# Kernel optimization log

Hardware: AMD Instinct MI355X
Metric: run time of the kernel (lower is better)

## Reference

```python
import jax, jax.numpy as jnp
import numpy as np

NT, NC = 100000, 25000
ETT, ECT = 800000, 400000
DIN_T, DIN_C = 64, 32
H, C = 4, 32
HID = H * C  # 128
SLOPE = 0.2  # GATConv LeakyReLU negative slope


def setup_inputs() -> dict:
    key = jax.random.key(0)
    ks = jax.random.split(key, 24)
    def p(i, shape, s=0.05):
        return jax.random.normal(ks[i], shape, dtype=jnp.float32) * s
    return {
        'x_target': jax.random.normal(ks[0], (NT, DIN_T), dtype=jnp.float32),
        'x_context': jax.random.normal(ks[1], (NC, DIN_C), dtype=jnp.float32),
        'edge_tt': jax.random.randint(ks[2], (2, ETT), 0, NT),
        'edge_ct_src': jax.random.randint(ks[3], (ECT,), 0, NC),
        'edge_ct_dst': jax.random.randint(ks[4], (ECT,), 0, NT),
        'W_pre_t': p(5, (DIN_T, HID)), 'b_pre_t': jnp.zeros((HID,), jnp.float32),
        'W_pre_c': p(6, (DIN_C, HID)), 'b_pre_c': jnp.zeros((HID,), jnp.float32),
        'W_sd': p(7, (HID, HID)), 'att_src_sd': p(8, (H, C)), 'att_dst_sd': p(9, (H, C)), 'b_sd': jnp.zeros((HID,), jnp.float32),
        'W_ds': p(10, (HID, HID)), 'att_src_ds': p(11, (H, C)), 'att_dst_ds': p(12, (H, C)), 'b_ds': jnp.zeros((HID,), jnp.float32),
        'W_ct_src': p(13, (HID, HID)), 'W_ct_dst': p(14, (HID, HID)), 'att_src_ct': p(15, (H, C)), 'att_dst_ct': p(16, (H, C)), 'b_ct': jnp.zeros((HID,), jnp.float32),
        'W_out': p(17, (HID, HID)), 'b_out': jnp.zeros((HID,), jnp.float32),
    }


def _gat(h_src, h_dst, att_s, att_d, src, dst, n_dst, bias):
    # h_src: [N_src,H,C] transformed src feats; h_dst: [N_dst,H,C]
    a_s = jnp.einsum('nhc,hc->nh', h_src, att_s)  # [N_src,H]
    a_d = jnp.einsum('nhc,hc->nh', h_dst, att_d)  # [N_dst,H]
    e = a_s[src] + a_d[dst]                        # [E,H]
    e = jnp.where(e > 0, e, SLOPE * e)             # LeakyReLU(0.2)
    m = jax.ops.segment_max(e, dst, num_segments=n_dst)  # stable softmax per dst
    ex = jnp.exp(e - m[dst])
    den = jax.ops.segment_sum(ex, dst, num_segments=n_dst)
    alpha = ex / den[dst]                          # [E,H]
    msg = h_src[src] * alpha[:, :, None]           # [E,H,C]
    out = jax.ops.segment_sum(msg, dst, num_segments=n_dst)
    return out.reshape(n_dst, H * C) + bias


def reference(x_target, x_context, edge_tt, edge_ct_src, edge_ct_dst,
              W_pre_t, b_pre_t, W_pre_c, b_pre_c,
              W_sd, att_src_sd, att_dst_sd, b_sd,
              W_ds, att_src_ds, att_dst_ds, b_ds,
              W_ct_src, W_ct_dst, att_src_ct, att_dst_ct, b_ct,
              W_out, b_out):
    # HeteroDictLinear pretransform + relu
    h_t = jax.nn.relu(x_target @ W_pre_t + b_pre_t)   # [NT,128]
    h_c = jax.nn.relu(x_context @ W_pre_c + b_pre_c)  # [NC,128]
    res = h_t
    # DirGATConv on (target,to,target): forward + reversed, each w/ self-loops
    loops = jnp.arange(NT)
    src_f = jnp.concatenate([edge_tt[0], loops]); dst_f = jnp.concatenate([edge_tt[1], loops])
    src_r = jnp.concatenate([edge_tt[1], loops]); dst_r = jnp.concatenate([edge_tt[0], loops])
    hs = (h_t @ W_sd).reshape(NT, H, C)
    out_sd = _gat(hs, hs, att_src_sd, att_dst_sd, src_f, dst_f, NT, b_sd)
    hd = (h_t @ W_ds).reshape(NT, H, C)
    out_ds = _gat(hd, hd, att_src_ds, att_dst_ds, src_r, dst_r, NT, b_ds)
    out_tt = 0.5 * out_sd + 0.5 * out_ds  # (1-alpha), alpha with alpha=0.5
    # bipartite GATConv on (context,to,target), no self loops
    hcs = (h_c @ W_ct_src).reshape(NC, H, C)
    htd = (h_t @ W_ct_dst).reshape(NT, H, C)
    out_ct = _gat(hcs, htd, att_src_ct, att_dst_ct, edge_ct_src, edge_ct_dst, NT, b_ct)
    # HeteroConv aggr='mean' over the two edge types hitting 'target'
    x = 0.5 * (out_tt + out_ct)
    x = jax.nn.relu(x + res)  # skip connection + relu
    return x @ W_out + b_out
```

## Files before the change

### kernel.cpp

```cpp
#include <hip/hip_runtime.h>
#include <cstdint>
#include <cstddef>

typedef unsigned short u16;
typedef unsigned int u32;

#define NT 100000
#define NC 25000
#define ETT 800000
#define ECT 400000
#define SLOPE 0.2f
#define LOG2E 1.4426950408889634f
#define OFFS (NT + 4)

#define NBK 782
#define NBLK 256
#define CHT ((ETT + NBLK - 1) / NBLK)
#define CHC ((ECT + NBLK - 1) / NBLK)
#define TOTC (3 * NBK * NBLK)
#define NSB ((TOTC + 4095) / 4096)
#define FILL_CAP 4096

#define PT_BLK ((NT + 63) / 64)
#define CT_BLK ((NC + 63) / 64)

typedef __attribute__((ext_vector_type(8))) short bf16x8;
typedef __attribute__((ext_vector_type(4))) float f32x4;

__device__ __forceinline__ u16 f2bf(float f) {
  u32 u = __float_as_uint(f);
  u32 r = (u >> 16) & 1u;
  return (u16)((u + 0x7fffu + r) >> 16);
}
__device__ __forceinline__ float lof(u32 p) { return __uint_as_float(p << 16); }
__device__ __forceinline__ float hif(u32 p) { return __uint_as_float(p & 0xffff0000u); }

__device__ __forceinline__ void compute_bpre(const int* __restrict__ bsum, int* s_bpre) {
  const int t = threadIdx.x;
  const int v = (t < NSB) ? bsum[t] : 0;
  s_bpre[t] = v;
  __syncthreads();
  for (int d = 1; d < 256; d <<= 1) {
    const int u = (t >= d) ? s_bpre[t - d] : 0;
    __syncthreads();
    s_bpre[t] += u;
    __syncthreads();
  }
  const int incl = s_bpre[t];
  __syncthreads();
  s_bpre[t] = incl - v;
  __syncthreads();
}

__global__ __launch_bounds__(256) void transform_hist_kernel(
    const int* __restrict__ tt_src, const int* __restrict__ tt_dst,
    const int* __restrict__ ect_d, int* __restrict__ cntblk,
    const float* __restrict__ Wsd, const float* __restrict__ AsSd, const float* __restrict__ AdSd,
    const float* __restrict__ Wds, const float* __restrict__ AsDs, const float* __restrict__ AdDs,
    const float* __restrict__ Wout,
    u16* __restrict__ bf_sd, u16* __restrict__ bf_ds, u16* __restrict__ bf_out,
    const float* __restrict__ Wcd, const float* __restrict__ attD,
    const float* __restrict__ bsd, const float* __restrict__ bds, const float* __restrict__ bct,
    float* __restrict__ cbias,
    const float* __restrict__ x_t, const float* __restrict__ Wpt, const float* __restrict__ bpt,
    u16* __restrict__ h_t, float* __restrict__ aD,
    const float* __restrict__ x_c, const float* __restrict__ Wpc, const float* __restrict__ bpc,
    const float* __restrict__ Wcs, const float* __restrict__ attS,
    u16* __restrict__ hc_bf, float* __restrict__ aS_c)
{
  __shared__ __align__(16) char smem[51200];
  const int t = threadIdx.x;

  if (blockIdx.x < NBLK) {
    int* h = (int*)smem;
    const int b = blockIdx.x;
    for (int i = t; i < 3 * NBK; i += 256) h[i] = 0;
    __syncthreads();
    const int lo = b * CHT, hi = min(lo + CHT, ETT);
    for (int i = lo + t; i < hi; i += 256) {
      atomicAdd(&h[tt_dst[i] >> 7], 1);
      atomicAdd(&h[NBK + (tt_src[i] >> 7)], 1);
    }
    const int lo2 = b * CHC, hi2 = min(lo2 + CHC, ECT);
    for (int i = lo2 + t; i < hi2; i += 256)
      atomicAdd(&h[2 * NBK + (ect_d[i] >> 7)], 1);
    __syncthreads();
    for (int i = t; i < 3 * NBK; i += 256)
      cntblk[(size_t)i * NBLK + b] = h[i];
    return;
  }

  const int b = blockIdx.x - NBLK;

  if (b < 4) {
    if (b == 3) {
      if (t < 128) cbias[t] = 0.25f * bsd[t] + 0.25f * bds[t] + 0.5f * bct[t];
      return;
    }
    float* fS = (float*)smem;
    float* fD = fS + 512;
    const float* W = (b == 0) ? Wsd : (b == 1) ? Wds : Wout;
    const float* As = (b == 0) ? AsSd : AsDs;
    const float* Ad = (b == 0) ? AdSd : AdDs;
    u16* out = (b == 0) ? bf_sd : (b == 1) ? bf_ds : bf_out;
    const int tiles = (b == 2) ? 8 : 9;
    if (b < 2) {
      if (t < 128) {
        for (int hh = 0; hh < 4; ++hh) {
          float s1 = 0.f, s2 = 0.f;
          for (int c = 0; c < 32; ++c) {
            const float wv = W[t * 128 + hh * 32 + c];
            s1 = fmaf(wv, As[hh * 32 + c], s1);
            s2 = fmaf(wv, Ad[hh * 32 + c], s2);
          }
          fS[t * 4 + hh] = s1 * LOG2E; fD[t * 4 + hh] = s2 * LOG2E;
        }
      }
      __syncthreads();
    }
    const int total = tiles * 4 * 64 * 8;
    for (int i = t; i < total; i += 256) {
      const int j = i & 7, lane = (i >> 3) & 63, ks = (i >> 9) & 3, ti = i >> 11;
      const int k = ks * 32 + (lane >> 4) * 8 + j;
      const int n = ti * 16 + (lane & 15);
      float v;
      if (n < 128) v = W[k * 128 + n];
      else if (n < 132) v = fS[k * 4 + (n - 128)];
      else if (n < 136) v = fD[k * 4 + (n - 132)];
      else v = 0.f;
      out[i] = f2bf(v);
    }
    return;
  }

  if (b < 4 + PT_BLK) {
    float (*s_xt)[68] = (float(*)[68])smem;
    float (*s_W)[128] = (float(*)[128])(smem + 17408);
    float* s_fold     = (float*)(smem + 17408 + 16384);
    const int row0 = (b - 4) * 64;
    for (int g = 0; g < 4; ++g) {
      const int lr = g * 16 + (t >> 4);
      const int k4 = (t & 15) * 4;
      const int grow = row0 + lr;
      float4 f = make_float4(0.f, 0.f, 0.f, 0.f);
      if (grow < NT) f = *(const float4*)(x_t + (size_t)grow * 64 + k4);
      s_xt[k4 + 0][lr] = f.x; s_xt[k4 + 1][lr] = f.y;
      s_xt[k4 + 2][lr] = f.z; s_xt[k4 + 3][lr] = f.w;
    }
    if (t < 128) {
      for (int hh = 0; hh < 4; ++hh) {
        float s = 0.f;
        for (int c = 0; c < 32; ++c)
          s = fmaf(Wcd[t * 128 + hh * 32 + c], attD[hh * 32 + c], s);
        s_fold[t * 4 + hh] = s * LOG2E;
      }
    }
    const int rg = t >> 4;
    const int cg = t & 15;
    float acc[4][8];
    for (int r = 0; r < 4; ++r)
      for (int j = 0; j < 8; ++j)
        acc[r][j] = bpt[cg * 4 + (j & 3) + (j >> 2) * 64];
    for (int kc = 0; kc < 64; kc += 32) {
      for (int j = 0; j < 4; ++j) {
        const int idx = t + j * 256;
        const int k = idx >> 5, c4 = (idx & 31) * 4;
        *(float4*)&s_W[k][c4] = *(const float4*)(Wpt + (size_t)(kc + k) * 128 + c4);
      }
      __syncthreads();
#pragma unroll 8
      for (int k = 0; k < 32; ++k) {
        const float4 xa = *(const float4*)&s_xt[kc + k][rg * 4];
        const float4 w0 = *(const float4*)&s_W[k][cg * 4];
        const float4 w1 = *(const float4*)&s_W[k][cg * 4 + 64];
        const float xr[4] = {xa.x, xa.y, xa.z, xa.w};
        for (int r = 0; r < 4; ++r) {
          acc[r][0] = fmaf(xr[r], w0.x, acc[r][0]);
          acc[r][1] = fmaf(xr[r], w0.y, acc[r][1]);
          acc[r][2] = fmaf(xr[r], w0.z, acc[r][2]);
          acc[r][3] = fmaf(xr[r], w0.w, acc[r][3]);
          acc[r][4] = fmaf(xr[r], w1.x, acc[r][4]);
          acc[r][5] = fmaf(xr[r], w1.y, acc[r][5]);
          acc[r][6] = fmaf(xr[r], w1.z, acc[r][6]);
          acc[r][7] = fmaf(xr[r], w1.w, acc[r][7]);
        }
      }
      __syncthreads();
    }
    float4 fc0[2], fc1[2];
    fc0[0] = *(const float4*)&s_fold[(cg * 4 + 0) * 4];
    (void)fc0; (void)fc1;
    for (int r = 0; r < 4; ++r) {
      const int grow = row0 + rg * 4 + r;
      float v[8];
      for (int j = 0; j < 8; ++j) v[j] = fmaxf(acc[r][j], 0.f);
      float p0 = 0.f, p1 = 0.f, p2 = 0.f, p3 = 0.f;
      for (int j = 0; j < 8; ++j) {
        const int col = cg * 4 + (j & 3) + ((j >> 2) * 64);
        const float4 f4 = *(const float4*)&s_fold[col * 4];
        p0 = fmaf(v[j], f4.x, p0); p1 = fmaf(v[j], f4.y, p1);
        p2 = fmaf(v[j], f4.z, p2); p3 = fmaf(v[j], f4.w, p3);
      }
      if (grow < NT) {
        uint2 pk;
        pk.x = (u32)f2bf(v[0]) | ((u32)f2bf(v[1]) << 16);
        pk.y = (u32)f2bf(v[2]) | ((u32)f2bf(v[3]) << 16);
        *(uint2*)(h_t + (size_t)grow * 128 + cg * 4) = pk;
        pk.x = (u32)f2bf(v[4]) | ((u32)f2bf(v[5]) << 16);
        pk.y = (u32)f2bf(v[6]) | ((u32)f2bf(v[7]) << 16);
        *(uint2*)(h_t + (size_t)grow * 128 + cg * 4 + 64) = pk;
      }
      for (int m = 1; m < 16; m <<= 1) {
        p0 += __shfl_xor(p0, m); p1 += __shfl_xor(p1, m);
        p2 += __shfl_xor(p2, m); p3 += __shfl_xor(p3, m);
      }
      if (cg == 0 && grow < NT)
        *(float4*)(aD + (size_t)grow * 4) = make_float4(p0, p1, p2, p3);
    }
    return;
  }

  {
    float (*s_ht)[68]  = (float(*)[68])smem;
    float (*s_W2)[128] = (float(*)[128])(smem + 34816);
    float (*s_xc)[68]  = (float(*)[68])smem;
    const int row0 = (b - 4 - PT_BLK) * 64;
    for (int g = 0; g < 2; ++g) {
      const int lr = g * 32 + (t >> 3);
      const int k4 = (t & 7) * 4;
      const int grow = row0 + lr;
      float4 f = make_float4(0.f, 0.f, 0.f, 0.f);
      if (grow < NC) f = *(const float4*)(x_c + (size_t)grow * 32 + k4);
      s_xc[k4 + 0][lr] = f.x; s_xc[k4 + 1][lr] = f.y;
      s_xc[k4 + 2][lr] = f.z; s_xc[k4 + 3][lr] = f.w;
    }
    for (int j = 0; j < 4; ++j) {
      const int idx = t + j * 256;
      const int k = idx >> 5, c4 = (idx & 31) * 4;
      *(float4*)&s_W2[k][c4] = *(const float4*)(Wpc + (size_t)k * 128 + c4);
    }
    __syncthreads();
    const int rg = t >> 4, cg = t & 15;
    float acc1[4][8];
    for (int r = 0; r < 4; ++r)
      for (int j = 0; j < 8; ++j)
        acc1[r][j] = bpc[cg * 4 + (j & 3) + (j >> 2) * 64];
#pragma unroll 8
    for (int k = 0; k < 32; ++k) {
      const float4 xa = *(const float4*)&s_xc[k][rg * 4];
      const float4 w0 = *(const float4*)&s_W2[k][cg * 4];
      const float4 w1 = *(const float4*)&s_W2[k][cg * 4 + 64];
      const float xr[4] = {xa.x, xa.y, xa.z, xa.w};
      for (int r = 0; r < 4; ++r) {
        acc1[r][0] = fmaf(xr[r], w0.x, acc1[r][0]);
        acc1[r][1] = fmaf(xr[r], w0.y, acc1[r][1]);
        acc1[r][2] = fmaf(xr[r], w0.z, acc1[r][2]);
        acc1[r][3] = fmaf(xr[r], w0.w, acc1[r][3]);
        acc1[r][4] = fmaf(xr[r], w1.x, acc1[r][4]);
        acc1[r][5] = fmaf(xr[r], w1.y, acc1[r][5]);
        acc1[r][6] = fmaf(xr[r], w1.z, acc1[r][6]);
        acc1[r][7] = fmaf(xr[r], w1.w, acc1[r][7]);
      }
    }
    __syncthreads();
    for (int r = 0; r < 4; ++r) {
      const int lr = rg * 4 + r;
      for (int j = 0; j < 8; ++j) {
        const int col = cg * 4 + (j & 3) + ((j >> 2) * 64);
        s_ht[col][lr] = fmaxf(acc1[r][j], 0.f);
      }
    }
    for (int j = 0; j < 4; ++j) {
      const int idx = t + j * 256;
      const int k = idx >> 5, c4 = (idx & 31) * 4;
      *(float4*)&s_W2[k][c4] = *(const float4*)(Wcs + (size_t)k * 128 + c4);
    }
    __syncthreads();
    float acc2[4][8];
    for (int r = 0; r < 4; ++r)
      for (int j = 0; j < 8; ++j) acc2[r][j] = 0.f;
    for (int kc = 0; kc < 128; kc += 32) {
#pragma unroll 8
      for (int k = 0; k < 32; ++k) {
        const float4 xa = *(const float4*)&s_ht[kc + k][rg * 4];
        const float4 w0 = *(const float4*)&s_W2[k][cg * 4];
        const float4 w1 = *(const float4*)&s_W2[k][cg * 4 + 64];
        const float xr[4] = {xa.x, xa.y, xa.z, xa.w};
        for (int r = 0; r < 4; ++r) {
          acc2[r][0] = fmaf(xr[r], w0.x, acc2[r][0]);
          acc2[r][1] = fmaf(xr[r], w0.y, acc2[r][1]);
          acc2[r][2] = fmaf(xr[r], w0.z, acc2[r][2]);
          acc2[r][3] = fmaf(xr[r], w0.w, acc2[r][3]);
          acc2[r][4] = fmaf(xr[r], w1.x, acc2[r][4]);
          acc2[r][5] = fmaf(xr[r], w1.y, acc2[r][5]);
          acc2[r][6] = fmaf(xr[r], w1.z, acc2[r][6]);
          acc2[r][7] = fmaf(xr[r], w1.w, acc2[r][7]);
        }
      }
      if (kc < 96) {
        __syncthreads();
        for (int j = 0; j < 4; ++j) {
          const int idx = t + j * 256;
          const int k = idx >> 5, c4 = (idx & 31) * 4;
          *(float4*)&s_W2[k][c4] = *(const float4*)(Wcs + (size_t)(kc + 32 + k) * 128 + c4);
        }
        __syncthreads();
      }
    }
    const int h2 = cg >> 3;
    const float4 at0 = *(const float4*)(attS + cg * 4);
    const float4 at1 = *(const float4*)(attS + cg * 4 + 64);
    for (int r = 0; r < 4; ++r) {
      const int grow = row0 + rg * 4 + r;
      float pa = acc2[r][0] * at0.x + acc2[r][1] * at0.y +
                 acc2[r][2] * at0.z + acc2[r][3] * at0.w;
      float pb = acc2[r][4] * at1.x + acc2[r][5] * at1.y +
                 acc2[r][6] * at1.z + acc2[r][7] * at1.w;
      if (grow < NC) {
        uint2 pk;
        pk.x = (u32)f2bf(acc2[r][0]) | ((u32)f2bf(acc2[r][1]) << 16);
        pk.y = (u32)f2bf(acc2[r][2]) | ((u32)f2bf(acc2[r][3]) << 16);
        *(uint2*)(hc_bf + (size_t)grow * 128 + cg * 4) = pk;
        pk.x = (u32)f2bf(acc2[r][4]) | ((u32)f2bf(acc2[r][5]) << 16);
        pk.y = (u32)f2bf(acc2[r][6]) | ((u32)f2bf(acc2[r][7]) << 16);
        *(uint2*)(hc_bf + (size_t)grow * 128 + cg * 4 + 64) = pk;
      }
      for (int m = 1; m < 8; m <<= 1) {
        pa += __shfl_xor(pa, m);
        pb += __shfl_xor(pb, m);
      }
      if ((cg & 7) == 0 && grow < NC) {
        aS_c[(size_t)grow * 4 + h2] = pa * LOG2E;
        aS_c[(size_t)grow * 4 + 2 + h2] = pb * LOG2E;
      }
    }
  }
}

__global__ __launch_bounds__(256) void scan2_blk_kernel(const int* __restrict__ in,
    int* __restrict__ out, int* __restrict__ bsum)
{
  const int t = threadIdx.x, b = blockIdx.x;
  const int idx = b * 4096 + t * 16;
  int v[16];
  int s = 0;
  if (idx < TOTC) {
#pragma unroll
    for (int q = 0; q < 4; ++q) {
      const int4 qq = *(const int4*)(in + idx + q * 4);
      v[q * 4 + 0] = s; s += qq.x;
      v[q * 4 + 1] = s; s += qq.y;
      v[q * 4 + 2] = s; s += qq.z;
      v[q * 4 + 3] = s; s += qq.w;
    }
  } else {
    for (int j = 0; j < 16; ++j) v[j] = 0;
  }
  __shared__ int sh[256];
  sh[t] = s;
  __syncthreads();
  for (int d = 1; d < 256; d <<= 1) {
    const int u = (t >= d) ? sh[t - d] : 0;
    __syncthreads();
    sh[t] += u;
    __syncthreads();
  }
  const int excl = (t == 0) ? 0 : sh[t - 1];
  if (idx < TOTC) {
#pragma unroll
    for (int q = 0; q < 4; ++q) {
      int4 qo;
      qo.x = excl + v[q * 4 + 0]; qo.y = excl + v[q * 4 + 1];
      qo.z = excl + v[q * 4 + 2]; qo.w = excl + v[q * 4 + 3];
      *(int4*)(out + idx + q * 4) = qo;
    }
  }
  if (t == 255) bsum[b] = sh[255];
}

__global__ __launch_bounds__(256) void bin_logits2_kernel(
    const int* __restrict__ tt_src, const int* __restrict__ tt_dst,
    const int* __restrict__ ect_s, const int* __restrict__ ect_d,
    const int* __restrict__ scanned, const int* __restrict__ bsum, u32* __restrict__ bin,
    const short* __restrict__ A, const short* __restrict__ Bsd, const short* __restrict__ Bds,
    u16* __restrict__ hs, float* __restrict__ aSsd, float* __restrict__ aDsd,
    u16* __restrict__ hd, float* __restrict__ aSds, float* __restrict__ aDds, int M)
{
  __shared__ __align__(16) float ldsf[4][16][148];
  const int t = threadIdx.x;

  if (blockIdx.x < NBLK) {
    int* cur = (int*)&ldsf[0][0][0];
    int* s_bpre = cur + 3 * NBK;
    compute_bpre(bsum, s_bpre);
    const int b = blockIdx.x;
    for (int i = t; i < 3 * NBK; i += 256) {
      const int idx = i * NBLK + b;
      cur[i] = scanned[idx] + s_bpre[idx >> 12];
    }
    __syncthreads();
    const int lo = b * CHT, hi = min(lo + CHT, ETT);
    for (int i = lo + t; i < hi; i += 256) {
      const int s = tt_src[i], d = tt_dst[i];
      int p = atomicAdd(&cur[d >> 7], 1);
      bin[p] = ((u32)(d & 127) << 17) | (u32)s;
      p = atomicAdd(&cur[NBK + (s >> 7)], 1);
      bin[p] = ((u32)(s & 127) << 17) | (u32)d;
    }
    const int lo2 = b * CHC, hi2 = min(lo2 + CHC, ECT);
    for (int i = lo2 + t; i < hi2; i += 256) {
      const int s = ect_s[i], d = ect_d[i];
      const int p = atomicAdd(&cur[2 * NBK + (d >> 7)], 1);
      bin[p] = ((u32)(d & 127) << 17) | (u32)s;
    }
    return;
  }

  float (*lds)[16][148] = ldsf;
  const int blk = blockIdx.x - NBLK;
  const int wv = t >> 6, lane = t & 63;
  const int quad = lane >> 4, l16 = lane & 15;
  const int row0 = blk * 64 + wv * 16;
  const int arow = min(row0 + l16, M - 1);
  const short* ap = A + (size_t)arow * 128 + quad * 8;
  bf16x8 af[4];
  for (int ks = 0; ks < 4; ++ks) af[ks] = *(const bf16x8*)(ap + ks * 32);
  const int row = row0 + l16;
  const int idx = lane & 7, rr = lane >> 3;
  for (int pass = 0; pass < 2; ++pass) {
    const short* B = pass ? Bds : Bsd;
    u16* outb = pass ? hd : hs;
    float* aS = pass ? aSds : aSsd;
    float* aD = pass ? aDds : aDsd;
    f32x4 acc[9];
    for (int ti = 0; ti < 9; ++ti) acc[ti] = (f32x4){0.f, 0.f, 0.f, 0.f};
    for (int ks = 0; ks < 4; ++ks)
      for (int ti = 0; ti < 9; ++ti) {
        const bf16x8 bf = *(const bf16x8*)(B + ((ti * 4 + ks) * 64 + lane) * 8);
        acc[ti] = __builtin_amdgcn_mfma_f32_16x16x32_bf16(af[ks], bf, acc[ti], 0, 0, 0);
      }
    for (int ti = 0; ti < 9; ++ti)
      for (int r = 0; r < 4; ++r)
        lds[wv][quad * 4 + r][ti * 16 + l16] = acc[ti][r];
    __syncthreads();
    if (row < M) {
      for (int g = 0; g < 8; ++g) {
        const f32x4 v = *(const f32x4*)&lds[wv][l16][g * 16 + quad * 4];
        uint2 pk;
        pk.x = (u32)f2bf(v[0]) | ((u32)f2bf(v[1]) << 16);
        pk.y = (u32)f2bf(v[2]) | ((u32)f2bf(v[3]) << 16);
        *(uint2*)(outb + (size_t)row * 128 + g * 16 + quad * 4) = pk;
      }
    }
    for (int p = 0; p < 2; ++p) {
      const int lr = p * 8 + rr;
      const int n = row0 + lr;
      if (n < M) {
        const float v = lds[wv][lr][128 + idx];
        if (idx < 4) aS[(size_t)n * 4 + idx] = v;
        else aD[(size_t)n * 4 + idx - 4] = v;
      }
    }
    __syncthreads();
  }
}

__global__ __launch_bounds__(256) void bucket_fill_kernel(const int* __restrict__ scanned,
    const int* __restrict__ bsum, const u32* __restrict__ bin,
    int* __restrict__ offs, int* __restrict__ big_el)
{
  __shared__ int s_cnt[128], s_exc[128], s_cur[128], s_bpre[256];
  __shared__ int s_el[FILL_CAP];
  const int t = threadIdx.x;
  compute_bpre(bsum, s_bpre);
  const int rel = blockIdx.x / NBK;
  const int bucket = blockIdx.x - rel * NBK;
  if (t < 128) s_cnt[t] = 0;
  const int bi = blockIdx.x * NBLK;
  const int base = scanned[bi] + s_bpre[bi >> 12];
  const int nxt = (blockIdx.x == 3 * NBK - 1)
                      ? (2 * ETT + ECT)
                      : scanned[bi + NBLK] + s_bpre[(bi + NBLK) >> 12];
  __syncthreads();
  const int size = nxt - base;
  for (int i = t; i < size; i += 256)
    atomicAdd(&s_cnt[bin[base + i] >> 17], 1);
  __syncthreads();
  if (t < 128) s_exc[t] = s_cnt[t];
  __syncthreads();
  for (int d = 1; d < 128; d <<= 1) {
    int v = 0;
    if (t < 128 && t >= d) v = s_exc[t - d];
    __syncthreads();
    if (t < 128) s_exc[t] += v;
    __syncthreads();
  }
  const int relbase = rel * ETT;
  const int obase = base - relbase;
  int* off_rel = offs + (size_t)rel * OFFS;
  const int node0 = bucket * 128;
  if (t < 128) {
    const int excl = s_exc[t] - s_cnt[t];
    s_cur[t] = excl;
    if (node0 + t < NT) off_rel[node0 + t] = obase + excl;
  }
  if (t == 0 && bucket == NBK - 1) off_rel[NT] = obase + size;
  __syncthreads();
  int* el_rel = big_el + relbase;
  if (size <= FILL_CAP) {
    for (int i = t; i < size; i += 256) {
      const u32 e = bin[base + i];
      const int pos = atomicAdd(&s_cur[e >> 17], 1);
      s_el[pos] = (int)(e & 0x1FFFFu);
    }
    __syncthreads();
    for (int i = t; i < size; i += 256)
      el_rel[obase + i] = s_el[i];
  } else {
    for (int i = t; i < size; i += 256) {
      const u32 e = bin[base + i];
      const int pos = atomicAdd(&s_cur[e >> 17], 1);
      el_rel[obase + pos] = (int)(e & 0x1FFFFu);
    }
  }
}

__global__ __launch_bounds__(256) void mfma_out_kernel(
    const short* __restrict__ A, const short* __restrict__ B,
    const float* __restrict__ bias, float* __restrict__ out, int M)
{
  __shared__ __align__(16) float lds[4][16][132];
  const int wv = threadIdx.x >> 6, lane = threadIdx.x & 63;
  const int quad = lane >> 4, l16 = lane & 15;
  const int row0 = blockIdx.x * 64 + wv * 16;
  const int arow = min(row0 + l16, M - 1);
  const short* ap = A + (size_t)arow * 128 + quad * 8;
  bf16x8 af[4];
  for (int ks = 0; ks < 4; ++ks) af[ks] = *(const bf16x8*)(ap + ks * 32);
  f32x4 acc[8];
  for (int t = 0; t < 8; ++t) acc[t] = (f32x4){0.f, 0.f, 0.f, 0.f};
  for (int ks = 0; ks < 4; ++ks)
    for (int t = 0; t < 8; ++t) {
      const bf16x8 bf = *(const bf16x8*)(B + ((t * 4 + ks) * 64 + lane) * 8);
      acc[t] = __builtin_amdgcn_mfma_f32_16x16x32_bf16(af[ks], bf, acc[t], 0, 0, 0);
    }
  for (int t = 0; t < 8; ++t)
    for (int r = 0; r < 4; ++r)
      lds[wv][quad * 4 + r][t * 16 + l16] = acc[t][r];
  __syncthreads();
  const int row = row0 + l16;
  if (row < M) {
    for (int g = 0; g < 8; ++g) {
      const int col = g * 16 + quad * 4;
      f32x4 v = *(const f32x4*)&lds[wv][l16][col];
      const f32x4 b4 = *(const f32x4*)(bias + col);
      v = v + b4;
      *(f32x4*)(out + (size_t)row * 128 + col) = v;
    }
  }
}

__device__ __forceinline__ void gat_pipe16(const int* __restrict__ off,
    const int* __restrict__ el, const float* __restrict__ aS, const float* __restrict__ aD,
    const u16* __restrict__ hb, int d, int h, int cb, int self_loop, float w,
    float* __restrict__ acc)
{
  const float ad = aD[(size_t)d * 4 + h];
  const int beg = off[d];
  const int m = off[d + 1] - beg;
  const int cnt = m + self_loop;
  if (cnt <= 0) return;
  float den = 0.f;
  float a0 = 0.f, a1 = 0.f, a2 = 0.f, a3 = 0.f, a4 = 0.f, a5 = 0.f, a6 = 0.f, a7 = 0.f;
  int sB = (1 < m) ? el[beg + 1] : d;
  {
    const int sA0 = (0 < m) ? el[beg] : d;
    float eA = aS[(size_t)sA0 * 4 + h];
    uint4 pA = *(const uint4*)(hb + (size_t)sA0 * 128 + cb);
    for (int k = 0; k < cnt; ++k) {
      const int sC = (k + 2 < m) ? el[beg + k + 2] : d;
      const float eB = aS[(size_t)sB * 4 + h];
      const uint4 pB = *(const uint4*)(hb + (size_t)sB * 128 + cb);
      float ea = eA + ad;
      ea = ea > 0.f ? ea : SLOPE * ea;
      const float ex = exp2f(ea);
      den += ex;
      a0 = fmaf(ex, lof(pA.x), a0); a1 = fmaf(ex, hif(pA.x), a1);
      a2 = fmaf(ex, lof(pA.y), a2); a3 = fmaf(ex, hif(pA.y), a3);
      a4 = fmaf(ex, lof(pA.z), a4); a5 = fmaf(ex, hif(pA.z), a5);
      a6 = fmaf(ex, lof(pA.w), a6); a7 = fmaf(ex, hif(pA.w), a7);
      eA = eB; pA = pB; sB = sC;
    }
  }
  const float s = w / den;
  acc[0] = fmaf(a0, s, acc[0]); acc[1] = fmaf(a1, s, acc[1]);
  acc[2] = fmaf(a2, s, acc[2]); acc[3] = fmaf(a3, s, acc[3]);
  acc[4] = fmaf(a4, s, acc[4]); acc[5] = fmaf(a5, s, acc[5]);
  acc[6] = fmaf(a6, s, acc[6]); acc[7] = fmaf(a7, s, acc[7]);
}

__global__ __launch_bounds__(256) void gather_all_kernel(
    const int* __restrict__ off_f, const int* __restrict__ el_f,
    const float* __restrict__ aS_sd, const float* __restrict__ aD_sd, const u16* __restrict__ hs,
    const int* __restrict__ off_r, const int* __restrict__ el_r,
    const float* __restrict__ aS_ds, const float* __restrict__ aD_ds, const u16* __restrict__ hd,
    const int* __restrict__ off_c, const int* __restrict__ el_c,
    const float* __restrict__ aS_ct, const float* __restrict__ aD_ct, const u16* __restrict__ hc,
    const u16* __restrict__ skip, const float* __restrict__ cbias, u16* __restrict__ x)
{
  const int d = blockIdx.x * 16 + (threadIdx.x >> 4);
  if (d >= NT) return;
  const int lg = threadIdx.x & 15;
  const int h = lg >> 2;
  const int cb = lg * 8;
  float acc[8];
  for (int i = 0; i < 8; ++i) acc[i] = 0.f;
  gat_pipe16(off_f, el_f, aS_sd, aD_sd, hs, d, h, cb, 1, 0.25f, acc);
  gat_pipe16(off_r, el_r, aS_ds, aD_ds, hd, d, h, cb, 1, 0.25f, acc);
  gat_pipe16(off_c, el_c, aS_ct, aD_ct, hc, d, h, cb, 0, 0.5f, acc);
  const uint4 sk = *(const uint4*)(skip + (size_t)d * 128 + cb);
  const float4 cb0 = *(const float4*)(cbias + cb);
  const float4 cb1 = *(const float4*)(cbias + cb + 4);
  const float o0 = fmaxf(acc[0] + cb0.x + lof(sk.x), 0.f);
  const float o1 = fmaxf(acc[1] + cb0.y + hif(sk.x), 0.f);
  const float o2 = fmaxf(acc[2] + cb0.z + lof(sk.y), 0.f);
  const float o3 = fmaxf(acc[3] + cb0.w + hif(sk.y), 0.f);
  const float o4 = fmaxf(acc[4] + cb1.x + lof(sk.z), 0.f);
  const float o5 = fmaxf(acc[5] + cb1.y + hif(sk.z), 0.f);
  const float o6 = fmaxf(acc[6] + cb1.z + lof(sk.w), 0.f);
  const float o7 = fmaxf(acc[7] + cb1.w + hif(sk.w), 0.f);
  uint4 r;
  r.x = (u32)f2bf(o0) | ((u32)f2bf(o1) << 16);
  r.y = (u32)f2bf(o2) | ((u32)f2bf(o3) << 16);
  r.z = (u32)f2bf(o4) | ((u32)f2bf(o5) << 16);
  r.w = (u32)f2bf(o6) | ((u32)f2bf(o7) << 16);
  *(uint4*)(x + (size_t)d * 128 + cb) = r;
}

extern "C" void kernel_launch(void* const* d_in, const int* in_sizes, int n_in,
                              void* d_out, int out_size, void* d_ws, size_t ws_size,
                              hipStream_t stream)
{
  const float* x_t   = (const float*)d_in[0];
  const float* x_c   = (const float*)d_in[1];
  const int*   e_tt  = (const int*)d_in[2];
  const int*   ect_s = (const int*)d_in[3];
  const int*   ect_d = (const int*)d_in[4];
  const float* Wpt = (const float*)d_in[5];   const float* bpt = (const float*)d_in[6];
  const float* Wpc = (const float*)d_in[7];   const float* bpc = (const float*)d_in[8];
  const float* Wsd = (const float*)d_in[9];   const float* As_sd = (const float*)d_in[10];
  const float* Ad_sd = (const float*)d_in[11]; const float* bsd = (const float*)d_in[12];
  const float* Wds = (const float*)d_in[13];  const float* As_ds = (const float*)d_in[14];
  const float* Ad_ds = (const float*)d_in[15]; const float* bds = (const float*)d_in[16];
  const float* Wcs = (const float*)d_in[17];  const float* Wcd = (const float*)d_in[18];
  const float* As_ct = (const float*)d_in[19]; const float* Ad_ct = (const float*)d_in[20];
  const float* bct = (const float*)d_in[21];
  const float* Wout = (const float*)d_in[22]; const float* bout = (const float*)d_in[23];

  char* p = (char*)d_ws;
  size_t off = 0;
  auto alloc = [&](size_t bytes) { char* r = p + off; off += (bytes + 255) & ~(size_t)255; return r; };
  u16* ht_bf   = (u16*)alloc((size_t)NT * 128 * 2);
  u16* hs_bf   = (u16*)alloc((size_t)NT * 128 * 2);
  u16* hd_bf   = (u16*)alloc((size_t)NT * 128 * 2);
  u16* hc_bf   = (u16*)alloc((size_t)NC * 128 * 2);
  u16* x_bf    = (u16*)alloc((size_t)NT * 128 * 2);
  float* aS_sd = (float*)alloc((size_t)NT * 4 * 4);
  float* aD_sd = (float*)alloc((size_t)NT * 4 * 4);
  float* aS_ds = (float*)alloc((size_t)NT * 4 * 4);
  float* aD_ds = (float*)alloc((size_t)NT * 4 * 4);
  float* aS_ct = (float*)alloc((size_t)NC * 4 * 4);
  float* aD_ct = (float*)alloc((size_t)NT * 4 * 4);
  int* cntblk  = (int*)alloc((size_t)TOTC * 4);
  int* scanned = (int*)alloc((size_t)TOTC * 4);
  u32* bin     = (u32*)alloc((size_t)(2 * ETT + ECT) * 4);
  int* big_el  = (int*)alloc((size_t)(2 * ETT + ECT) * 4);
  int* offs    = (int*)alloc((size_t)3 * OFFS * 4);
  int* bsum    = (int*)alloc((size_t)NSB * 4);
  float* cbias   = (float*)alloc(128 * 4);
  u16* bfrag_sd  = (u16*)alloc((size_t)9 * 4 * 64 * 8 * 2);
  u16* bfrag_ds  = (u16*)alloc((size_t)9 * 4 * 64 * 8 * 2);
  u16* bfrag_out = (u16*)alloc((size_t)8 * 4 * 64 * 8 * 2);

  int* off_f = offs;
  int* off_r = offs + OFFS;
  int* off_c = offs + 2 * OFFS;
  int* el_f = big_el;
  int* el_r = big_el + ETT;
  int* el_c = big_el + 2 * ETT;

  const int* tt_src = e_tt;
  const int* tt_dst = e_tt + ETT;

  const int gM = (NT + 63) / 64;

  transform_hist_kernel<<<NBLK + 4 + PT_BLK + CT_BLK, 256, 0, stream>>>(
      tt_src, tt_dst, ect_d, cntblk,
      Wsd, As_sd, Ad_sd, Wds, As_ds, Ad_ds, Wout,
      bfrag_sd, bfrag_ds, bfrag_out,
      Wcd, Ad_ct, bsd, bds, bct, cbias,
      x_t, Wpt, bpt, ht_bf, aD_ct,
      x_c, Wpc, bpc, Wcs, As_ct, hc_bf, aS_ct);

  scan2_blk_kernel<<<NSB, 256, 0, stream>>>(cntblk, scanned, bsum);

  bin_logits2_kernel<<<NBLK + gM, 256, 0, stream>>>(
      tt_src, tt_dst, ect_s, ect_d, scanned, bsum, bin,
      (const short*)ht_bf, (const short*)bfrag_sd, (const short*)bfrag_ds,
      hs_bf, aS_sd, aD_sd, hd_bf, aS_ds, aD_ds, NT);

  bucket_fill_kernel<<<3 * NBK, 256, 0, stream>>>(scanned, bsum, bin, offs, big_el);

  gather_all_kernel<<<(NT + 15) / 16, 256, 0, stream>>>(
      off_f, el_f, aS_sd, aD_sd, hs_bf,
      off_r, el_r, aS_ds, aD_ds, hd_bf,
      off_c, el_c, aS_ct, aD_ct, hc_bf,
      ht_bf, cbias, x_bf);

  mfma_out_kernel<<<gM, 256, 0, stream>>>((const short*)x_bf, (const short*)bfrag_out,
                                          bout, (float*)d_out, NT);
}
```

Before: 375.7 us.

## Shrink LDS in transform kernel, halve context tiles, drop LDS from output GEMM

Cuts the transform kernel's shared memory from 51200 to 27648 bytes. It does this by streaming weights in 16-row K chunks and processing context nodes in 32-row tiles instead of 64, which should let more blocks fit per CU. The output MFMA kernel now writes accumulators straight to global memory with the bias added, instead of staging them through LDS with a barrier. The trade-offs are more syncthreads per block, twice as many context blocks, and narrower strided stores in the output kernel.

```diff
diff --git a/kernel.cpp b/kernel.cpp
--- a/kernel.cpp
+++ b/kernel.cpp
@@ -22,7 +22,8 @@
 #define FILL_CAP 4096
 
 #define PT_BLK ((NT + 63) / 64)
-#define CT_BLK ((NC + 63) / 64)
+#define CT_BLK ((NC + 31) / 32)
+#define GM_BLK ((NT + 63) / 64)
 
 typedef __attribute__((ext_vector_type(8))) short bf16x8;
 typedef __attribute__((ext_vector_type(4))) float f32x4;
@@ -68,7 +69,7 @@
     const float* __restrict__ Wcs, const float* __restrict__ attS,
     u16* __restrict__ hc_bf, float* __restrict__ aS_c)
 {
-  __shared__ __align__(16) char smem[51200];
+  __shared__ __align__(16) char smem[27648];
   const int t = threadIdx.x;
 
   if (blockIdx.x < NBLK) {
@@ -136,7 +137,7 @@
   if (b < 4 + PT_BLK) {
     float (*s_xt)[68] = (float(*)[68])smem;
     float (*s_W)[128] = (float(*)[128])(smem + 17408);
-    float* s_fold     = (float*)(smem + 17408 + 16384);
+    float* s_fold     = (float*)(smem + 17408 + 8192);
     const int row0 = (b - 4) * 64;
     for (int g = 0; g < 4; ++g) {
       const int lr = g * 16 + (t >> 4);
@@ -161,15 +162,15 @@
     for (int r = 0; r < 4; ++r)
       for (int j = 0; j < 8; ++j)
         acc[r][j] = bpt[cg * 4 + (j & 3) + (j >> 2) * 64];
-    for (int kc = 0; kc < 64; kc += 32) {
-      for (int j = 0; j < 4; ++j) {
+    for (int kc = 0; kc < 64; kc += 16) {
+      for (int j = 0; j < 2; ++j) {
         const int idx = t + j * 256;
         const int k = idx >> 5, c4 = (idx & 31) * 4;
         *(float4*)&s_W[k][c4] = *(const float4*)(Wpt + (size_t)(kc + k) * 128 + c4);
       }
       __syncthreads();
-#pragma unroll 8
-      for (int k = 0; k < 32; ++k) {
+#pragma unroll
+      for (int k = 0; k < 16; ++k) {
         const float4 xa = *(const float4*)&s_xt[kc + k][rg * 4];
         const float4 w0 = *(const float4*)&s_W[k][cg * 4];
         const float4 w1 = *(const float4*)&s_W[k][cg * 4 + 64];
@@ -187,9 +188,6 @@
       }
       __syncthreads();
     }
-    float4 fc0[2], fc1[2];
-    fc0[0] = *(const float4*)&s_fold[(cg * 4 + 0) * 4];
-    (void)fc0; (void)fc1;
     for (int r = 0; r < 4; ++r) {
       const int grow = row0 + rg * 4 + r;
       float v[8];
@@ -221,12 +219,12 @@
   }
 
   {
-    float (*s_ht)[68]  = (float(*)[68])smem;
-    float (*s_W2)[128] = (float(*)[128])(smem + 34816);
-    float (*s_xc)[68]  = (float(*)[68])smem;
-    const int row0 = (b - 4 - PT_BLK) * 64;
-    for (int g = 0; g < 2; ++g) {
-      const int lr = g * 32 + (t >> 3);
+    float (*s_ht)[36]  = (float(*)[36])smem;
+    float (*s_W2)[128] = (float(*)[128])(smem + 18432);
+    float (*s_xc)[36]  = (float(*)[36])smem;
+    const int row0 = (b - 4 - PT_BLK) * 32;
+    {
+      const int lr = t >> 3;
       const int k4 = (t & 7) * 4;
       const int grow = row0 + lr;
       float4 f = make_float4(0.f, 0.f, 0.f, 0.f);
@@ -234,59 +232,61 @@
       s_xc[k4 + 0][lr] = f.x; s_xc[k4 + 1][lr] = f.y;
       s_xc[k4 + 2][lr] = f.z; s_xc[k4 + 3][lr] = f.w;
     }
-    for (int j = 0; j < 4; ++j) {
-      const int idx = t + j * 256;
-      const int k = idx >> 5, c4 = (idx & 31) * 4;
-      *(float4*)&s_W2[k][c4] = *(const float4*)(Wpc + (size_t)k * 128 + c4);
-    }
-    __syncthreads();
     const int rg = t >> 4, cg = t & 15;
-    float acc1[4][8];
-    for (int r = 0; r < 4; ++r)
+    float acc1[2][8];
+    for (int r = 0; r < 2; ++r)
       for (int j = 0; j < 8; ++j)
         acc1[r][j] = bpc[cg * 4 + (j & 3) + (j >> 2) * 64];
-#pragma unroll 8
-    for (int k = 0; k < 32; ++k) {
-      const float4 xa = *(const float4*)&s_xc[k][rg * 4];
-      const float4 w0 = *(const float4*)&s_W2[k][cg * 4];
-      const float4 w1 = *(const float4*)&s_W2[k][cg * 4 + 64];
-      const float xr[4] = {xa.x, xa.y, xa.z, xa.w};
-      for (int r = 0; r < 4; ++r) {
-        acc1[r][0] = fmaf(xr[r], w0.x, acc1[r][0]);
-        acc1[r][1] = fmaf(xr[r], w0.y, acc1[r][1]);
-        acc1[r][2] = fmaf(xr[r], w0.z, acc1[r][2]);
-        acc1[r][3] = fmaf(xr[r], w0.w, acc1[r][3]);
-        acc1[r][4] = fmaf(xr[r], w1.x, acc1[r][4]);
-        acc1[r][5] = fmaf(xr[r], w1.y, acc1[r][5]);
-        acc1[r][6] = fmaf(xr[r], w1.z, acc1[r][6]);
-        acc1[r][7] = fmaf(xr[r], w1.w, acc1[r][7]);
-      }
-    }
-    __syncthreads();
-    for (int r = 0; r < 4; ++r) {
-      const int lr = rg * 4 + r;
+    for (int kc = 0; kc < 32; kc += 16) {
+      for (int j = 0; j < 2; ++j) {
+        const int idx = t + j * 256;
+        const int k = idx >> 5, c4 = (idx & 31) * 4;
+        *(float4*)&s_W2[k][c4] = *(const float4*)(Wpc + (size_t)(kc + k) * 128 + c4);
+      }
+      __syncthreads();
+#pragma unroll
+      for (int k = 0; k < 16; ++k) {
+        const float2 xa = *(const float2*)&s_xc[kc + k][rg * 2];
+        const float4 w0 = *(const float4*)&s_W2[k][cg * 4];
+        const float4 w1 = *(const float4*)&s_W2[k][cg * 4 + 64];
+        const float xr[2] = {xa.x, xa.y};
+        for (int r = 0; r < 2; ++r) {
+          acc1[r][0] = fmaf(xr[r], w0.x, acc1[r][0]);
+          acc1[r][1] = fmaf(xr[r], w0.y, acc1[r][1]);
+          acc1[r][2] = fmaf(xr[r], w0.z, acc1[r][2]);
+          acc1[r][3] = fmaf(xr[r], w0.w, acc1[r][3]);
+          acc1[r][4] = fmaf(xr[r], w1.x, acc1[r][4]);
+          acc1[r][5] = fmaf(xr[r], w1.y, acc1[r][5]);
+          acc1[r][6] = fmaf(xr[r], w1.z, acc1[r][6]);
+          acc1[r][7] = fmaf(xr[r], w1.w, acc1[r][7]);
+        }
+      }
+      __syncthreads();
+    }
+    for (int r = 0; r < 2; ++r) {
+      const int lr = rg * 2 + r;
       for (int j = 0; j < 8; ++j) {
         const int col = cg * 4 + (j & 3) + ((j >> 2) * 64);
         s_ht[col][lr] = fmaxf(acc1[r][j], 0.f);
       }
     }
-    for (int j = 0; j < 4; ++j) {
-      const int idx = t + j * 256;
-      const int k = idx >> 5, c4 = (idx & 31) * 4;
-      *(float4*)&s_W2[k][c4] = *(const float4*)(Wcs + (size_t)k * 128 + c4);
-    }
-    __syncthreads();
-    float acc2[4][8];
-    for (int r = 0; r < 4; ++r)
+    float acc2[2][8];
+    for (int r = 0; r < 2; ++r)
       for (int j = 0; j < 8; ++j) acc2[r][j] = 0.f;
-    for (int kc = 0; kc < 128; kc += 32) {
-#pragma unroll 8
-      for (int k = 0; k < 32; ++k) {
-        const float4 xa = *(const float4*)&s_ht[kc + k][rg * 4];
+    for (int kc = 0; kc < 128; kc += 16) {
+      for (int j = 0; j < 2; ++j) {
+        const int idx = t + j * 256;
+        const int k = idx >> 5, c4 = (idx & 31) * 4;
+        *(float4*)&s_W2[k][c4] = *(const float4*)(Wcs + (size_t)(kc + k) * 128 + c4);
+      }
+      __syncthreads();
+#pragma unroll
+      for (int k = 0; k < 16; ++k) {
+        const float2 xa = *(const float2*)&s_ht[kc + k][rg * 2];
         const float4 w0 = *(const float4*)&s_W2[k][cg * 4];
         const float4 w1 = *(const float4*)&s_W2[k][cg * 4 + 64];
-        const float xr[4] = {xa.x, xa.y, xa.z, xa.w};
-        for (int r = 0; r < 4; ++r) {
+        const float xr[2] = {xa.x, xa.y};
+        for (int r = 0; r < 2; ++r) {
           acc2[r][0] = fmaf(xr[r], w0.x, acc2[r][0]);
           acc2[r][1] = fmaf(xr[r], w0.y, acc2[r][1]);
           acc2[r][2] = fmaf(xr[r], w0.z, acc2[r][2]);
@@ -297,21 +297,13 @@
           acc2[r][7] = fmaf(xr[r], w1.w, acc2[r][7]);
         }
       }
-      if (kc < 96) {
-        __syncthreads();
-        for (int j = 0; j < 4; ++j) {
-          const int idx = t + j * 256;
-          const int k = idx >> 5, c4 = (idx & 31) * 4;
-          *(float4*)&s_W2[k][c4] = *(const float4*)(Wcs + (size_t)(kc + 32 + k) * 128 + c4);
-        }
-        __syncthreads();
-      }
+      __syncthreads();
     }
     const int h2 = cg >> 3;
     const float4 at0 = *(const float4*)(attS + cg * 4);
     const float4 at1 = *(const float4*)(attS + cg * 4 + 64);
-    for (int r = 0; r < 4; ++r) {
-      const int grow = row0 + rg * 4 + r;
+    for (int r = 0; r < 2; ++r) {
+      const int grow = row0 + rg * 2 + r;
       float pa = acc2[r][0] * at0.x + acc2[r][1] * at0.y +
                  acc2[r][2] * at0.z + acc2[r][3] * at0.w;
       float pb = acc2[r][4] * at1.x + acc2[r][5] * at1.y +
@@ -378,46 +370,12 @@
   if (t == 255) bsum[b] = sh[255];
 }
 
-__global__ __launch_bounds__(256) void bin_logits2_kernel(
-    const int* __restrict__ tt_src, const int* __restrict__ tt_dst,
-    const int* __restrict__ ect_s, const int* __restrict__ ect_d,
-    const int* __restrict__ scanned, const int* __restrict__ bsum, u32* __restrict__ bin,
+__device__ __forceinline__ void logits2_body(float (*lds)[16][148], int blk,
     const short* __restrict__ A, const short* __restrict__ Bsd, const short* __restrict__ Bds,
     u16* __restrict__ hs, float* __restrict__ aSsd, float* __restrict__ aDsd,
     u16* __restrict__ hd, float* __restrict__ aSds, float* __restrict__ aDds, int M)
 {
-  __shared__ __align__(16) float ldsf[4][16][148];
   const int t = threadIdx.x;
-
-  if (blockIdx.x < NBLK) {
-    int* cur = (int*)&ldsf[0][0][0];
-    int* s_bpre = cur + 3 * NBK;
-    compute_bpre(bsum, s_bpre);
-    const int b = blockIdx.x;
-    for (int i = t; i < 3 * NBK; i += 256) {
-      const int idx = i * NBLK + b;
-      cur[i] = scanned[idx] + s_bpre[idx >> 12];
-    }
-    __syncthreads();
-    const int lo = b * CHT, hi = min(lo + CHT, ETT);
-    for (int i = lo + t; i < hi; i += 256) {
-      const int s = tt_src[i], d = tt_dst[i];
-      int p = atomicAdd(&cur[d >> 7], 1);
-      bin[p] = ((u32)(d & 127) << 17) | (u32)s;
-      p = atomicAdd(&cur[NBK + (s >> 7)], 1);
-      bin[p] = ((u32)(s & 127) << 17) | (u32)d;
-    }
-    const int lo2 = b * CHC, hi2 = min(lo2 + CHC, ECT);
-    for (int i = lo2 + t; i < hi2; i += 256) {
-      const int s = ect_s[i], d = ect_d[i];
-      const int p = atomicAdd(&cur[2 * NBK + (d >> 7)], 1);
-      bin[p] = ((u32)(d & 127) << 17) | (u32)s;
-    }
-    return;
-  }
-
-  float (*lds)[16][148] = ldsf;
-  const int blk = blockIdx.x - NBLK;
   const int wv = t >> 6, lane = t & 63;
   const int quad = lane >> 4, l16 = lane & 15;
   const int row0 = blk * 64 + wv * 16;
@@ -463,6 +421,47 @@
     }
     __syncthreads();
   }
+}
+
+__global__ __launch_bounds__(256) void bin_logits2_kernel(
+    const int* __restrict__ tt_src, const int* __restrict__ tt_dst,
+    const int* __restrict__ ect_s, const int* __restrict__ ect_d,
+    const int* __restrict__ scanned, const int* __restrict__ bsum, u32* __restrict__ bin,
+    const short* __restrict__ A, const short* __restrict__ Bsd, const short* __restrict__ Bds,
+    u16* __restrict__ hs, float* __restrict__ aSsd, float* __restrict__ aDsd,
+    u16* __restrict__ hd, float* __restrict__ aSds, float* __restrict__ aDds, int M)
+{
+  __shared__ __align__(16) float ldsf[4][16][148];
+  const int t = threadIdx.x;
+
+  if (blockIdx.x < NBLK) {
+    int* cur = (int*)&ldsf[0][0][0];
+    int* s_bpre = cur + 3 * NBK;
+    compute_bpre(bsum, s_bpre);
+    const int b = blockIdx.x;
+    for (int i = t; i < 3 * NBK; i += 256) {
+      const int idx = i * NBLK + b;
+      cur[i] = scanned[idx] + s_bpre[idx >> 12];
+    }
+    __syncthreads();
+    const int lo = b * CHT, hi = min(lo + CHT, ETT);
+    for (int i = lo + t; i < hi; i += 256) {
+      const int s = tt_src[i], d = tt_dst[i];
+      int p = atomicAdd(&cur[d >> 7], 1);
+      bin[p] = ((u32)(d & 127) << 17) | (u32)s;
+      p = atomicAdd(&cur[NBK + (s >> 7)], 1);
+      bin[p] = ((u32)(s & 127) << 17) | (u32)d;
+    }
+    const int lo2 = b * CHC, hi2 = min(lo2 + CHC, ECT);
+    for (int i = lo2 + t; i < hi2; i += 256) {
+      const int s = ect_s[i], d = ect_d[i];
+      const int p = atomicAdd(&cur[2 * NBK + (d >> 7)], 1);
+      bin[p] = ((u32)(d & 127) << 17) | (u32)s;
+    }
+    return;
+  }
+  logits2_body(ldsf, blockIdx.x - NBLK, A, Bsd, Bds,
+               hs, aSsd, aDsd, hd, aSds, aDds, M);
 }
 
 __global__ __launch_bounds__(256) void bucket_fill_kernel(const int* __restrict__ scanned,
@@ -529,33 +528,32 @@
     const short* __restrict__ A, const short* __restrict__ B,
     const float* __restrict__ bias, float* __restrict__ out, int M)
 {
-  __shared__ __align__(16) float lds[4][16][132];
-  const int wv = threadIdx.x >> 6, lane = threadIdx.x & 63;
+  const int t = threadIdx.x;
+  const int wv = t >> 6, lane = t & 63;
   const int quad = lane >> 4, l16 = lane & 15;
-  const int row0 = blockIdx.x * 64 + wv * 16;
-  const int arow = min(row0 + l16, M - 1);
+  const int r0 = blockIdx.x * 64 + wv * 16;
+  const int arow = min(r0 + l16, M - 1);
   const short* ap = A + (size_t)arow * 128 + quad * 8;
   bf16x8 af[4];
   for (int ks = 0; ks < 4; ++ks) af[ks] = *(const bf16x8*)(ap + ks * 32);
   f32x4 acc[8];
-  for (int t = 0; t < 8; ++t) acc[t] = (f32x4){0.f, 0.f, 0.f, 0.f};
+  for (int ti = 0; ti < 8; ++ti) acc[ti] = (f32x4){0.f, 0.f, 0.f, 0.f};
   for (int ks = 0; ks < 4; ++ks)
-    for (int t = 0; t < 8; ++t) {
-      const bf16x8 bf = *(const bf16x8*)(B + ((t * 4 + ks) * 64 + lane) * 8);
-      acc[t] = __builtin_amdgcn_mfma_f32_16x16x32_bf16(af[ks], bf, acc[t], 0, 0, 0);
-    }
-  for (int t = 0; t < 8; ++t)
-    for (int r = 0; r < 4; ++r)
-      lds[wv][quad * 4 + r][t * 16 + l16] = acc[t][r];
-  __syncthreads();
-  const int row = row0 + l16;
-  if (row < M) {
-    for (int g = 0; g < 8; ++g) {
-      const int col = g * 16 + quad * 4;
-      f32x4 v = *(const f32x4*)&lds[wv][l16][col];
-      const f32x4 b4 = *(const f32x4*)(bias + col);
-      v = v + b4;
-      *(f32x4*)(out + (size_t)row * 128 + col) = v;
+    for (int ti = 0; ti < 8; ++ti) {
+      const bf16x8 bf = *(const bf16x8*)(B + ((ti * 4 + ks) * 64 + lane) * 8);
+      acc[ti] = __builtin_amdgcn_mfma_f32_16x16x32_bf16(af[ks], bf, acc[ti], 0, 0, 0);
+    }
+  float bcol[8];
+#pragma unroll
+  for (int ti = 0; ti < 8; ++ti) bcol[ti] = bias[ti * 16 + l16];
+#pragma unroll
+  for (int r = 0; r < 4; ++r) {
+    const int row = r0 + quad * 4 + r;
+    if (row < M) {
+      float* orow = out + (size_t)row * 128 + l16;
+#pragma unroll
+      for (int ti = 0; ti < 8; ++ti)
+        orow[ti * 16] = acc[ti][r] + bcol[ti];
     }
   }
 }
@@ -692,8 +690,6 @@
   const int* tt_src = e_tt;
   const int* tt_dst = e_tt + ETT;
 
-  const int gM = (NT + 63) / 64;
-
   transform_hist_kernel<<<NBLK + 4 + PT_BLK + CT_BLK, 256, 0, stream>>>(
       tt_src, tt_dst, ect_d, cntblk,
       Wsd, As_sd, Ad_sd, Wds, As_ds, Ad_ds, Wout,
@@ -704,7 +700,7 @@
 
   scan2_blk_kernel<<<NSB, 256, 0, stream>>>(cntblk, scanned, bsum);
 
-  bin_logits2_kernel<<<NBLK + gM, 256, 0, stream>>>(
+  bin_logits2_kernel<<<NBLK + GM_BLK, 256, 0, stream>>>(
       tt_src, tt_dst, ect_s, ect_d, scanned, bsum, bin,
       (const short*)ht_bf, (const short*)bfrag_sd, (const short*)bfrag_ds,
       hs_bf, aS_sd, aD_sd, hd_bf, aS_ds, aD_ds, NT);
@@ -717,6 +713,6 @@
       off_c, el_c, aS_ct, aD_ct, hc_bf,
       ht_bf, cbias, x_bf);
 
-  mfma_out_kernel<<<gM, 256, 0, stream>>>((const short*)x_bf, (const short*)bfrag_out,
-                                          bout, (float*)d_out, NT);
-}
+  mfma_out_kernel<<<GM_BLK, 256, 0, stream>>>((const short*)x_bf, (const short*)bfrag_out,
+                                              bout, (float*)d_out, NT);
+}
```

Result: no change. 381.9 us (+1.6%).
